# Kernel tuning notes

Measured on AMD Instinct MI355X. Metric: run time of the kernel, lower is better.

The kernel has to match this reference:

```python
import jax, jax.numpy as jnp
import numpy as np

D_MODEL = 256
D_INNER = 512   # expand=2
D_STATE = 16
D_CONV = 4
DT_RANK = 16    # ceil(d_model/16)
EPS = 1e-5


def _ln(x, g, b):
    m = x.mean(-1, keepdims=True)
    v = jnp.mean((x - m) ** 2, -1, keepdims=True)
    return (x - m) * jax.lax.rsqrt(v + EPS) * g + b


def _mamba(x, W_in, conv_w, conv_b, W_x, W_dt, b_dt, A_log, Dp, W_out):
    B, N, _ = x.shape
    xz = x @ W_in.T                               # [B,N,2*Di]
    xs, z = jnp.split(xz, 2, axis=-1)
    # depthwise causal conv1d, kernel D_CONV, left pad D_CONV-1
    xp = jnp.pad(xs, ((0, 0), (D_CONV - 1, 0), (0, 0)))
    xc = sum(xp[:, k:k + N, :] * conv_w[:, k] for k in range(D_CONV)) + conv_b
    xc = jax.nn.silu(xc)                          # [B,N,Di]
    dbl = xc @ W_x.T                              # [B,N,dt_rank+2*S]
    dt, Bm, Cm = jnp.split(dbl, [DT_RANK, DT_RANK + D_STATE], axis=-1)
    dt = jax.nn.softplus(dt @ W_dt.T + b_dt)      # [B,N,Di]
    A = -jnp.exp(A_log)                           # [Di,S]
    dA = jnp.exp(dt[..., None] * A)               # [B,N,Di,S]
    dBx = dt[..., None] * Bm[:, :, None, :] * xc[..., None]

    def step(h, inp):
        dA_t, dBx_t, c_t = inp                    # [B,Di,S],[B,Di,S],[B,S]
        h = dA_t * h + dBx_t
        y = jnp.einsum('bds,bs->bd', h, c_t)
        return h, y

    h0 = jnp.zeros((B, D_INNER, D_STATE), xs.dtype)
    _, ys = jax.lax.scan(step, h0, (dA.swapaxes(0, 1), dBx.swapaxes(0, 1), Cm.swapaxes(0, 1)))
    y = ys.swapaxes(0, 1) + Dp * xc
    y = y * jax.nn.silu(z)
    return y @ W_out.T                            # [B,N,d_model]


def setup_inputs() -> dict:
    key = jax.random.key(0)
    ks = jax.random.split(key, 24)
    g = lambda k, s, sc=0.02: jax.random.normal(k, s, jnp.float32) * sc
    inp = {}
    inp['input_states'] = jax.random.normal(ks[0], (1, 8192, D_MODEL), jnp.float32)
    inp['position_states'] = jax.random.normal(ks[1], (1, 8192, D_MODEL), jnp.float32)
    inp['W_in'] = g(ks[2], (2 * D_INNER, D_MODEL))
    inp['conv_w'] = g(ks[3], (D_INNER, D_CONV), 0.2)
    inp['conv_b'] = jnp.zeros((D_INNER,), jnp.float32)
    inp['W_x'] = g(ks[4], (DT_RANK + 2 * D_STATE, D_INNER))
    inp['W_dt'] = g(ks[5], (D_INNER, DT_RANK), 0.1)
    inp['b_dt'] = g(ks[6], (D_INNER,), 0.1)
    # S4D-real init: A_log = log(1..d_state) broadcast over channels
    inp['A_log'] = jnp.log(jnp.broadcast_to(jnp.arange(1, D_STATE + 1, dtype=jnp.float32), (D_INNER, D_STATE)))
    inp['Dp'] = jnp.ones((D_INNER,), jnp.float32)
    inp['W_out'] = g(ks[7], (D_MODEL, D_INNER))
    inp['W_lin'] = g(ks[8], (D_MODEL, D_MODEL))
    inp['b_lin'] = jnp.zeros((D_MODEL,), jnp.float32)
    inp['ln1_g'] = jnp.ones((D_MODEL,), jnp.float32)
    inp['ln1_b'] = jnp.zeros((D_MODEL,), jnp.float32)
    inp['W_exp'] = g(ks[9], (2 * D_MODEL, D_MODEL))
    inp['b_exp'] = jnp.zeros((2 * D_MODEL,), jnp.float32)
    inp['W_sq'] = g(ks[10], (D_MODEL, 2 * D_MODEL))
    inp['b_sq'] = jnp.zeros((D_MODEL,), jnp.float32)
    inp['ln2_g'] = jnp.ones((D_MODEL,), jnp.float32)
    inp['ln2_b'] = jnp.zeros((D_MODEL,), jnp.float32)
    return inp


def reference(input_states, position_states, W_in, conv_w, conv_b, W_x, W_dt, b_dt,
              A_log, Dp, W_out, W_lin, b_lin, ln1_g, ln1_b, W_exp, b_exp, W_sq, b_sq,
              ln2_g, ln2_b):
    h = _mamba(input_states, W_in, conv_w, conv_b, W_x, W_dt, b_dt, A_log, Dp, W_out)
    h = h @ W_lin.T + b_lin
    h = _ln(h + input_states, ln1_g, ln1_b)
    ff = jax.nn.relu(h @ W_exp.T + b_exp) @ W_sq.T + b_sq
    out = _ln(h + ff, ln2_g, ln2_b)
    # RPEMamba returns (hidden, input_states) as (states, attention_scores)
    return out, input_states
```

## Files before the change

### kernel.cpp

```cpp
#include <hip/hip_runtime.h>
#include <stdint.h>

#define NT 8192
#define DM 256
#define DI 512
#define DS 16
#define DR 16
#define NCH 256
#define LCH 32
#define NSUP 16
#define CPS 16

typedef __bf16 bf16_t;
typedef bf16_t bf16x8 __attribute__((ext_vector_type(8)));
typedef float f32x4 __attribute__((ext_vector_type(4)));

__device__ __forceinline__ unsigned short f2b(float f) {
    union { float f; unsigned int i; } v; v.f = f;
    unsigned int r = v.i + 0x7fffu + ((v.i >> 16) & 1u);
    return (unsigned short)(r >> 16);
}
__device__ __forceinline__ bf16x8 ld_frag_lds(const unsigned short* p) {
    union { uint4 u; bf16x8 b; } v;
    v.u = *(const uint4*)p;
    return v.b;
}
__device__ __forceinline__ void async16(const unsigned short* g, unsigned short* l) {
    __builtin_amdgcn_global_load_lds(
        (const __attribute__((address_space(1))) unsigned int*)g,
        (__attribute__((address_space(3))) unsigned int*)l, 16, 0, 0);
}

struct CvtArgs {
    const float* src[7];
    unsigned short* dst[7];
    int cnt[7];
    int total;
};
__global__ __launch_bounds__(256) void cvt_all(CvtArgs a) {
    int i = blockIdx.x * 256 + threadIdx.x;
    if (i >= a.total) return;
    #pragma unroll
    for (int s = 0; s < 7; s++) {
        if (i < a.cnt[s]) { a.dst[s][i] = f2b(a.src[s][i]); return; }
        i -= a.cnt[s];
    }
}

template<int BM, int BN, int FLAGS>
__global__ __launch_bounds__(256) void gemm_lds(
    const unsigned short* __restrict__ A, const unsigned short* __restrict__ B,
    int M, int N, int K,
    const float* __restrict__ bias, const float* __restrict__ resid,
    float* __restrict__ Cf, unsigned short* __restrict__ Cb)
{
    constexpr int MI = BM / 32;
    constexpr int NJ = BN / 32;
    __shared__ unsigned short sA[BM * 64];
    __shared__ unsigned short sB[BN * 64];
    const int tid = threadIdx.x;
    const int m0 = blockIdx.x * BM;
    const int n0 = blockIdx.y * BN;
    const int wave = tid >> 6, lane = tid & 63;
    const int wm = (wave & 1) * (BM / 2);
    const int wn = (wave >> 1) * (BN / 2);
    const int qm = lane >> 4, rm = lane & 15;

    f32x4 acc[MI][NJ];
    #pragma unroll
    for (int i = 0; i < MI; i++)
        #pragma unroll
        for (int j = 0; j < NJ; j++)
            #pragma unroll
            for (int r = 0; r < 4; r++) acc[i][j][r] = 0.f;

    const int sr = tid >> 3;
    const int sc = (tid & 7) * 8;

    for (int k0 = 0; k0 < K; k0 += 64) {
        __syncthreads();
        #pragma unroll
        for (int j = 0; j < BM / 32; j++) {
            int r = sr + j * 32;
            async16(A + (size_t)(m0 + r) * K + k0 + sc, &sA[r * 64 + sc]);
        }
        #pragma unroll
        for (int j = 0; j < BN / 32; j++) {
            int r = sr + j * 32;
            if (n0 + r < N)
                async16(B + (size_t)(n0 + r) * K + k0 + sc, &sB[r * 64 + sc]);
        }
        __syncthreads();
        #pragma unroll
        for (int ks = 0; ks < 64; ks += 32) {
            bf16x8 af[MI], bfr[NJ];
            #pragma unroll
            for (int i = 0; i < MI; i++)
                af[i] = ld_frag_lds(&sA[(wm + i * 16 + rm) * 64 + ks + qm * 8]);
            #pragma unroll
            for (int j = 0; j < NJ; j++)
                bfr[j] = ld_frag_lds(&sB[(wn + j * 16 + rm) * 64 + ks + qm * 8]);
            #pragma unroll
            for (int i = 0; i < MI; i++)
                #pragma unroll
                for (int j = 0; j < NJ; j++)
                    acc[i][j] = __builtin_amdgcn_mfma_f32_16x16x32_bf16(
                        af[i], bfr[j], acc[i][j], 0, 0, 0);
        }
    }

    #pragma unroll
    for (int i = 0; i < MI; i++) {
        int mrow = m0 + wm + i * 16 + qm * 4;
        #pragma unroll
        for (int j = 0; j < NJ; j++) {
            int ncol = n0 + wn + j * 16 + rm;
            if (ncol < N) {
                #pragma unroll
                for (int r = 0; r < 4; r++) {
                    float v = acc[i][j][r];
                    int mm = mrow + r;
                    if constexpr (FLAGS & 1) v += bias[ncol];
                    if constexpr (FLAGS & 4) v += resid[(size_t)mm * N + ncol];
                    if constexpr (FLAGS & 2) v = v > 0.f ? v : 0.f;
                    if constexpr (FLAGS & 8) Cf[(size_t)mm * N + ncol] = v;
                    if constexpr (FLAGS & 16) Cb[(size_t)mm * N + ncol] = f2b(v);
                }
            }
        }
    }
}

__global__ __launch_bounds__(256) void conv_silu(
    const float* __restrict__ xz, const float* __restrict__ cw,
    const float* __restrict__ cb, float* __restrict__ xc,
    unsigned short* __restrict__ xcb)
{
    int idx = blockIdx.x * 256 + threadIdx.x;
    int d = idx & (DI - 1), t = idx >> 9;
    float v = cb[d];
    #pragma unroll
    for (int k = 0; k < 4; k++) {
        int tt = t - 3 + k;
        if (tt >= 0) v += xz[(size_t)tt * 1024 + d] * cw[d * 4 + k];
    }
    float s = v / (1.f + __expf(-v));
    xc[idx] = s;
    xcb[idx] = f2b(s);
}

__global__ __launch_bounds__(256) void scan1(
    const float* __restrict__ dbl, const float* __restrict__ Wdt,
    const float* __restrict__ bdt, const float* __restrict__ xc,
    const float* __restrict__ A_log, float* __restrict__ dt,
    float* __restrict__ Ac, float* __restrict__ Bc)
{
    __shared__ float sD[LCH][DR];
    __shared__ float sB[LCH][DS];
    const int d = blockIdx.x * 256 + threadIdx.x;
    const int c = blockIdx.y;
    const int t0 = c * LCH;
    for (int e = threadIdx.x; e < LCH * 32; e += 256) {
        int tt = e >> 5, col = e & 31;
        float v = dbl[(size_t)(t0 + tt) * 48 + col];
        if (col < DR) sD[tt][col] = v; else sB[tt][col - DR] = v;
    }
    __syncthreads();
    float w[DR];
    #pragma unroll
    for (int j = 0; j < DR; j++) w[j] = Wdt[d * DR + j];
    const float bd = bdt[d];
    float A[DS], h[DS];
    #pragma unroll
    for (int s = 0; s < DS; s++) { A[s] = -__expf(A_log[d * DS + s]); h[s] = 0.f; }
    float sumdt = 0.f;
    for (int t = 0; t < LCH; t++) {
        float accd = bd;
        #pragma unroll
        for (int j = 0; j < DR; j++) accd += sD[t][j] * w[j];
        float dtv = accd > 20.f ? accd : log1pf(__expf(accd));
        dt[(size_t)(t0 + t) * DI + d] = dtv;
        float xcv = xc[(size_t)(t0 + t) * DI + d];
        float dtx = dtv * xcv;
        sumdt += dtv;
        #pragma unroll
        for (int s = 0; s < DS; s++)
            h[s] = __expf(dtv * A[s]) * h[s] + dtx * sB[t][s];
    }
    #pragma unroll
    for (int s = 0; s < DS; s++) {
        size_t off = ((size_t)c * DS + s) * DI + d;
        Ac[off] = __expf(sumdt * A[s]);
        Bc[off] = h[s];
    }
}

__global__ __launch_bounds__(256) void scan2a(
    const float* __restrict__ Ac, const float* __restrict__ Bc,
    float* __restrict__ Ap, float* __restrict__ Hl,
    float* __restrict__ Es, float* __restrict__ Ds)
{
    int p = blockIdx.x * 256 + threadIdx.x;
    int j = blockIdx.y;
    float h = 0.f, P = 1.f;
    for (int cc = 0; cc < CPS; cc++) {
        size_t off = (size_t)(j * CPS + cc) * 8192 + p;
        Hl[off] = h; Ap[off] = P;
        float a = Ac[off];
        h = a * h + Bc[off];
        P *= a;
    }
    Es[(size_t)j * 8192 + p] = h;
    Ds[(size_t)j * 8192 + p] = P;
}

__global__ __launch_bounds__(256) void scan2b(
    const float* __restrict__ Es, const float* __restrict__ Ds,
    float* __restrict__ Ss)
{
    int p = blockIdx.x * 256 + threadIdx.x;
    float S = 0.f;
    for (int j = 0; j < NSUP; j++) {
        Ss[(size_t)j * 8192 + p] = S;
        S = Ds[(size_t)j * 8192 + p] * S + Es[(size_t)j * 8192 + p];
    }
}

__global__ __launch_bounds__(256) void scan3(
    const float* __restrict__ dt, const float* __restrict__ xc,
    const float* __restrict__ xz, const float* __restrict__ dbl,
    const float* __restrict__ A_log, const float* __restrict__ Dp,
    const float* __restrict__ Ap, const float* __restrict__ Hl,
    const float* __restrict__ Ss, unsigned short* __restrict__ ygb)
{
    __shared__ float sB[LCH][DS];
    __shared__ float sC[LCH][DS];
    const int d = blockIdx.x * 256 + threadIdx.x;
    const int c = blockIdx.y;
    const int jsup = c >> 4;
    const int t0 = c * LCH;
    for (int e = threadIdx.x; e < LCH * 32; e += 256) {
        int tt = e >> 5, col = e & 31;
        float v = dbl[(size_t)(t0 + tt) * 48 + DR + col];
        if (col < DS) sB[tt][col] = v; else sC[tt][col - DS] = v;
    }
    __syncthreads();
    float A[DS], h[DS];
    #pragma unroll
    for (int s = 0; s < DS; s++) {
        A[s] = -__expf(A_log[d * DS + s]);
        size_t off = (size_t)c * 8192 + s * DI + d;
        h[s] = Ap[off] * Ss[(size_t)jsup * 8192 + s * DI + d] + Hl[off];
    }
    float dpv = Dp[d];
    for (int t = 0; t < LCH; t++) {
        float dtv = dt[(size_t)(t0 + t) * DI + d];
        float xcv = xc[(size_t)(t0 + t) * DI + d];
        float zv  = xz[(size_t)(t0 + t) * 1024 + DI + d];
        float dtx = dtv * xcv;
        float y = 0.f;
        #pragma unroll
        for (int s = 0; s < DS; s++) {
            h[s] = __expf(dtv * A[s]) * h[s] + dtx * sB[t][s];
            y += h[s] * sC[t][s];
        }
        float sz = zv / (1.f + __expf(-zv));
        ygb[(size_t)(t0 + t) * DI + d] = f2b((y + dpv * xcv) * sz);
    }
}

__global__ __launch_bounds__(256) void lnorm(
    const float* __restrict__ X, const float* __restrict__ X2,
    const float* __restrict__ g, const float* __restrict__ b,
    float* __restrict__ outf, unsigned short* __restrict__ outb)
{
    int wave = threadIdx.x >> 6, lane = threadIdx.x & 63;
    int row = blockIdx.x * 4 + wave;
    const float* x = X + (size_t)row * DM;
    float v[4];
    #pragma unroll
    for (int i = 0; i < 4; i++) {
        int col = lane + i * 64;
        v[i] = x[col];
        if (X2) v[i] += X2[(size_t)row * DM + col];
    }
    float s = v[0] + v[1] + v[2] + v[3];
    float s2 = v[0]*v[0] + v[1]*v[1] + v[2]*v[2] + v[3]*v[3];
    #pragma unroll
    for (int m = 1; m < 64; m <<= 1) {
        s  += __shfl_xor(s, m, 64);
        s2 += __shfl_xor(s2, m, 64);
    }
    float mean = s * (1.f / DM);
    float var = s2 * (1.f / DM) - mean * mean;
    float inv = rsqrtf(var + 1e-5f);
    #pragma unroll
    for (int i = 0; i < 4; i++) {
        int col = lane + i * 64;
        float o = (v[i] - mean) * inv * g[col] + b[col];
        if (outf) outf[(size_t)row * DM + col] = o;
        if (outb) outb[(size_t)row * DM + col] = f2b(o);
    }
}

static constexpr size_t OFF_XZ    = 0;
static constexpr size_t OFF_XC    = 33554432;
static constexpr size_t OFF_XCB   = 50331648;
static constexpr size_t OFF_DBL   = 58720256;
static constexpr size_t OFF_DT    = 60293120;
static constexpr size_t OFF_AC    = 77070336;
static constexpr size_t OFF_BC    = 85458944;
static constexpr size_t OFF_HL    = 93847552;
static constexpr size_t OFF_AP    = 102236160;
static constexpr size_t OFF_YGB   = 110624768;
static constexpr size_t OFF_XB    = 119013376;
static constexpr size_t OFF_ES    = 123207680;
static constexpr size_t OFF_DS2   = 123731968;
static constexpr size_t OFF_SS    = 124256256;
static constexpr size_t OFF_WINB  = 124780544;
static constexpr size_t OFF_WXB   = 125304832;
static constexpr size_t OFF_WOUTB = 125353984;
static constexpr size_t OFF_WLINB = 125616128;
static constexpr size_t OFF_WEXPB = 125747200;
static constexpr size_t OFF_WSQB  = 126009344;
static constexpr size_t OFF_H1B   = OFF_XZ;
static constexpr size_t OFF_H2    = OFF_XZ + 4194304;
static constexpr size_t OFF_HLN   = OFF_XZ + 12582912;
static constexpr size_t OFF_HLNB  = OFF_XZ + 20971520;
static constexpr size_t OFF_FF1B  = OFF_DT;
static constexpr size_t OFF_FF2   = OFF_DT + 8388608;

extern "C" void kernel_launch(void* const* d_in, const int* in_sizes, int n_in,
                              void* d_out, int out_size, void* d_ws, size_t ws_size,
                              hipStream_t stream)
{
    const float* x      = (const float*)d_in[0];
    const float* W_in   = (const float*)d_in[2];
    const float* conv_w = (const float*)d_in[3];
    const float* conv_b = (const float*)d_in[4];
    const float* W_x    = (const float*)d_in[5];
    const float* W_dt   = (const float*)d_in[6];
    const float* b_dt   = (const float*)d_in[7];
    const float* A_log  = (const float*)d_in[8];
    const float* Dp     = (const float*)d_in[9];
    const float* W_out  = (const float*)d_in[10];
    const float* W_lin  = (const float*)d_in[11];
    const float* b_lin  = (const float*)d_in[12];
    const float* ln1_g  = (const float*)d_in[13];
    const float* ln1_b  = (const float*)d_in[14];
    const float* W_exp  = (const float*)d_in[15];
    const float* b_exp  = (const float*)d_in[16];
    const float* W_sq   = (const float*)d_in[17];
    const float* b_sq   = (const float*)d_in[18];
    const float* ln2_g  = (const float*)d_in[19];
    const float* ln2_b  = (const float*)d_in[20];

    char* ws = (char*)d_ws;
    float* xz   = (float*)(ws + OFF_XZ);
    float* xc   = (float*)(ws + OFF_XC);
    unsigned short* xcb = (unsigned short*)(ws + OFF_XCB);
    float* dbl  = (float*)(ws + OFF_DBL);
    float* dtf  = (float*)(ws + OFF_DT);
    float* Ac   = (float*)(ws + OFF_AC);
    float* Bc   = (float*)(ws + OFF_BC);
    float* Hl   = (float*)(ws + OFF_HL);
    float* Ap   = (float*)(ws + OFF_AP);
    float* Es   = (float*)(ws + OFF_ES);
    float* Ds   = (float*)(ws + OFF_DS2);
    float* Ss   = (float*)(ws + OFF_SS);
    unsigned short* ygb   = (unsigned short*)(ws + OFF_YGB);
    unsigned short* xb    = (unsigned short*)(ws + OFF_XB);
    unsigned short* winb  = (unsigned short*)(ws + OFF_WINB);
    unsigned short* wxb   = (unsigned short*)(ws + OFF_WXB);
    unsigned short* woutb = (unsigned short*)(ws + OFF_WOUTB);
    unsigned short* wlinb = (unsigned short*)(ws + OFF_WLINB);
    unsigned short* wexpb = (unsigned short*)(ws + OFF_WEXPB);
    unsigned short* wsqb  = (unsigned short*)(ws + OFF_WSQB);
    unsigned short* h1b   = (unsigned short*)(ws + OFF_H1B);
    float* h2   = (float*)(ws + OFF_H2);
    float* hln  = (float*)(ws + OFF_HLN);
    unsigned short* hlnb  = (unsigned short*)(ws + OFF_HLNB);
    unsigned short* ff1b  = (unsigned short*)(ws + OFF_FF1B);
    float* ff2  = (float*)(ws + OFF_FF2);
    float* outp = (float*)d_out;

    CvtArgs ca;
    ca.src[0] = x;     ca.dst[0] = xb;    ca.cnt[0] = NT * DM;
    ca.src[1] = W_in;  ca.dst[1] = winb;  ca.cnt[1] = 1024 * DM;
    ca.src[2] = W_x;   ca.dst[2] = wxb;   ca.cnt[2] = 48 * DI;
    ca.src[3] = W_out; ca.dst[3] = woutb; ca.cnt[3] = DM * DI;
    ca.src[4] = W_lin; ca.dst[4] = wlinb; ca.cnt[4] = DM * DM;
    ca.src[5] = W_exp; ca.dst[5] = wexpb; ca.cnt[5] = DI * DM;
    ca.src[6] = W_sq;  ca.dst[6] = wsqb;  ca.cnt[6] = DM * DI;
    ca.total = ca.cnt[0]+ca.cnt[1]+ca.cnt[2]+ca.cnt[3]+ca.cnt[4]+ca.cnt[5]+ca.cnt[6];
    cvt_all<<<(ca.total + 255) / 256, 256, 0, stream>>>(ca);

    gemm_lds<128,128,8><<<dim3(64, 8), 256, 0, stream>>>(xb, winb, NT, 1024, DM,
                                                         nullptr, nullptr, xz, nullptr);
    conv_silu<<<NT * DI / 256, 256, 0, stream>>>(xz, conv_w, conv_b, xc, xcb);
    gemm_lds<128,64,8><<<dim3(64, 1), 256, 0, stream>>>(xcb, wxb, NT, 48, DI,
                                                        nullptr, nullptr, dbl, nullptr);
    scan1<<<dim3(2, NCH), 256, 0, stream>>>(dbl, W_dt, b_dt, xc, A_log, dtf, Ac, Bc);
    scan2a<<<dim3(32, NSUP), 256, 0, stream>>>(Ac, Bc, Ap, Hl, Es, Ds);
    scan2b<<<32, 256, 0, stream>>>(Es, Ds, Ss);
    scan3<<<dim3(2, NCH), 256, 0, stream>>>(dtf, xc, xz, dbl, A_log, Dp, Ap, Hl, Ss, ygb);
    gemm_lds<64,128,16><<<dim3(128, 2), 256, 0, stream>>>(ygb, woutb, NT, DM, DI,
                                                          nullptr, nullptr, nullptr, h1b);
    gemm_lds<64,128,1|4|8><<<dim3(128, 2), 256, 0, stream>>>(h1b, wlinb, NT, DM, DM,
                                                             b_lin, x, h2, nullptr);
    lnorm<<<NT / 4, 256, 0, stream>>>(h2, nullptr, ln1_g, ln1_b, hln, hlnb);
    gemm_lds<128,128,1|2|16><<<dim3(64, 4), 256, 0, stream>>>(hlnb, wexpb, NT, DI, DM,
                                                              b_exp, nullptr, nullptr, ff1b);
    gemm_lds<64,128,1|8><<<dim3(128, 2), 256, 0, stream>>>(ff1b, wsqb, NT, DM, DI,
                                                           b_sq, nullptr, ff2, nullptr);
    lnorm<<<NT / 4, 256, 0, stream>>>(hln, ff2, ln2_g, ln2_b, outp, nullptr);
    hipMemcpyAsync(outp + (size_t)NT * DM, x, (size_t)NT * DM * sizeof(float),
                   hipMemcpyDeviceToDevice, stream);
}
```

Baseline: 292.0 us.

## Recompute conv/dt inside scan kernels, halve chunk length, fold output copy into layernorm

The scan kernels now recompute the causal conv+SiLU and the dt projection/softplus from xz and dbl instead of reading fp32 xc and dt buffers, which removes those intermediate arrays and their global traffic. Chunk length drops from 32 to 16, doubling the number of chunks and super-chunks, which gives more parallel blocks but makes the scan2 stages longer. The passthrough copy of input_states is moved into the final layernorm kernel, replacing a separate memcpy. The cost is redundant arithmetic in both scan passes and larger Ac/Bc/Hl/Ap buffers.

Result: no change. 289.4 us (-0.9%).

```diff
diff --git a/kernel.cpp b/kernel.cpp
--- a/kernel.cpp
+++ b/kernel.cpp
@@ -6,9 +6,9 @@
 #define DI 512
 #define DS 16
 #define DR 16
-#define NCH 256
-#define LCH 32
-#define NSUP 16
+#define NCH 512
+#define LCH 16
+#define NSUP 32
 #define CPS 16
 
 typedef __bf16 bf16_t;
@@ -29,6 +29,12 @@
     __builtin_amdgcn_global_load_lds(
         (const __attribute__((address_space(1))) unsigned int*)g,
         (__attribute__((address_space(3))) unsigned int*)l, 16, 0, 0);
+}
+__device__ __forceinline__ float fast_softplus(float x) {
+    return x > 20.f ? x : __logf(1.f + __expf(x));
+}
+__device__ __forceinline__ float silu(float x) {
+    return x / (1.f + __expf(-x));
 }
 
 struct CvtArgs {
@@ -131,10 +137,9 @@
     }
 }
 
-__global__ __launch_bounds__(256) void conv_silu(
+__global__ __launch_bounds__(256) void conv_silu_b(
     const float* __restrict__ xz, const float* __restrict__ cw,
-    const float* __restrict__ cb, float* __restrict__ xc,
-    unsigned short* __restrict__ xcb)
+    const float* __restrict__ cb, unsigned short* __restrict__ xcb)
 {
     int idx = blockIdx.x * 256 + threadIdx.x;
     int d = idx & (DI - 1), t = idx >> 9;
@@ -144,48 +149,59 @@
         int tt = t - 3 + k;
         if (tt >= 0) v += xz[(size_t)tt * 1024 + d] * cw[d * 4 + k];
     }
-    float s = v / (1.f + __expf(-v));
-    xc[idx] = s;
-    xcb[idx] = f2b(s);
-}
-
-__global__ __launch_bounds__(256) void scan1(
-    const float* __restrict__ dbl, const float* __restrict__ Wdt,
-    const float* __restrict__ bdt, const float* __restrict__ xc,
-    const float* __restrict__ A_log, float* __restrict__ dt,
+    xcb[idx] = f2b(silu(v));
+}
+
+__global__ __launch_bounds__(256, 4) void scan1(
+    const float* __restrict__ xz, const float* __restrict__ cw,
+    const float* __restrict__ cbp, const float* __restrict__ dbl,
+    const float* __restrict__ Wdt, const float* __restrict__ bdt,
+    const float* __restrict__ A_log,
     float* __restrict__ Ac, float* __restrict__ Bc)
 {
-    __shared__ float sD[LCH][DR];
-    __shared__ float sB[LCH][DS];
+    __shared__ float sR[LCH * 48];
     const int d = blockIdx.x * 256 + threadIdx.x;
     const int c = blockIdx.y;
     const int t0 = c * LCH;
-    for (int e = threadIdx.x; e < LCH * 32; e += 256) {
-        int tt = e >> 5, col = e & 31;
-        float v = dbl[(size_t)(t0 + tt) * 48 + col];
-        if (col < DR) sD[tt][col] = v; else sB[tt][col - DR] = v;
+    {
+        const float4* src = (const float4*)(dbl + (size_t)t0 * 48);
+        if (threadIdx.x < 192) ((float4*)sR)[threadIdx.x] = src[threadIdx.x];
     }
     __syncthreads();
-    float w[DR];
+    const float cw0 = cw[d*4], cw1 = cw[d*4+1], cw2 = cw[d*4+2], cw3 = cw[d*4+3];
+    const float cb = cbp[d];
+    const float* xzp = xz + d;
+    float x0 = (t0 >= 3) ? xzp[(size_t)(t0-3) * 1024] : 0.f;
+    float x1 = (t0 >= 2) ? xzp[(size_t)(t0-2) * 1024] : 0.f;
+    float x2 = (t0 >= 1) ? xzp[(size_t)(t0-1) * 1024] : 0.f;
+    float w[DR], A[DS], h[DS];
     #pragma unroll
     for (int j = 0; j < DR; j++) w[j] = Wdt[d * DR + j];
     const float bd = bdt[d];
-    float A[DS], h[DS];
     #pragma unroll
     for (int s = 0; s < DS; s++) { A[s] = -__expf(A_log[d * DS + s]); h[s] = 0.f; }
     float sumdt = 0.f;
+    #pragma unroll 4
     for (int t = 0; t < LCH; t++) {
+        float x3 = xzp[(size_t)(t0 + t) * 1024];
+        float cv = cb + x0 * cw0 + x1 * cw1 + x2 * cw2 + x3 * cw3;
+        x0 = x1; x1 = x2; x2 = x3;
+        float xcv = silu(cv);
+        const float* r = &sR[t * 48];
+        float4 rd[4], rb[4];
+        #pragma unroll
+        for (int k = 0; k < 4; k++) { rd[k] = ((const float4*)r)[k]; rb[k] = ((const float4*)r)[4 + k]; }
         float accd = bd;
         #pragma unroll
-        for (int j = 0; j < DR; j++) accd += sD[t][j] * w[j];
-        float dtv = accd > 20.f ? accd : log1pf(__expf(accd));
-        dt[(size_t)(t0 + t) * DI + d] = dtv;
-        float xcv = xc[(size_t)(t0 + t) * DI + d];
+        for (int k = 0; k < 4; k++)
+            accd += rd[k].x * w[4*k] + rd[k].y * w[4*k+1] + rd[k].z * w[4*k+2] + rd[k].w * w[4*k+3];
+        float dtv = fast_softplus(accd);
+        sumdt += dtv;
         float dtx = dtv * xcv;
-        sumdt += dtv;
+        const float* bptr = (const float*)rb;
         #pragma unroll
         for (int s = 0; s < DS; s++)
-            h[s] = __expf(dtv * A[s]) * h[s] + dtx * sB[t][s];
+            h[s] = __expf(dtv * A[s]) * h[s] + dtx * bptr[s];
     }
     #pragma unroll
     for (int s = 0; s < DS; s++) {
@@ -226,53 +242,80 @@
     }
 }
 
-__global__ __launch_bounds__(256) void scan3(
-    const float* __restrict__ dt, const float* __restrict__ xc,
-    const float* __restrict__ xz, const float* __restrict__ dbl,
-    const float* __restrict__ A_log, const float* __restrict__ Dp,
+__global__ __launch_bounds__(256, 4) void scan3(
+    const float* __restrict__ xz, const float* __restrict__ cw,
+    const float* __restrict__ cbp, const float* __restrict__ dbl,
+    const float* __restrict__ Wdt, const float* __restrict__ bdt,
+    const float* __restrict__ A_log, const float* __restrict__ Dpp,
     const float* __restrict__ Ap, const float* __restrict__ Hl,
     const float* __restrict__ Ss, unsigned short* __restrict__ ygb)
 {
-    __shared__ float sB[LCH][DS];
-    __shared__ float sC[LCH][DS];
+    __shared__ float sR[LCH * 48];
     const int d = blockIdx.x * 256 + threadIdx.x;
     const int c = blockIdx.y;
-    const int jsup = c >> 4;
+    const int jsup = c / CPS;
     const int t0 = c * LCH;
-    for (int e = threadIdx.x; e < LCH * 32; e += 256) {
-        int tt = e >> 5, col = e & 31;
-        float v = dbl[(size_t)(t0 + tt) * 48 + DR + col];
-        if (col < DS) sB[tt][col] = v; else sC[tt][col - DS] = v;
+    {
+        const float4* src = (const float4*)(dbl + (size_t)t0 * 48);
+        if (threadIdx.x < 192) ((float4*)sR)[threadIdx.x] = src[threadIdx.x];
     }
     __syncthreads();
-    float A[DS], h[DS];
+    const float cw0 = cw[d*4], cw1 = cw[d*4+1], cw2 = cw[d*4+2], cw3 = cw[d*4+3];
+    const float cb = cbp[d];
+    const float* xzp = xz + d;
+    const float* zp  = xz + DI + d;
+    float x0 = (t0 >= 3) ? xzp[(size_t)(t0-3) * 1024] : 0.f;
+    float x1 = (t0 >= 2) ? xzp[(size_t)(t0-2) * 1024] : 0.f;
+    float x2 = (t0 >= 1) ? xzp[(size_t)(t0-1) * 1024] : 0.f;
+    float w[DR], A[DS], h[DS];
+    #pragma unroll
+    for (int j = 0; j < DR; j++) w[j] = Wdt[d * DR + j];
+    const float bd = bdt[d];
+    const float dpv = Dpp[d];
     #pragma unroll
     for (int s = 0; s < DS; s++) {
         A[s] = -__expf(A_log[d * DS + s]);
         size_t off = (size_t)c * 8192 + s * DI + d;
         h[s] = Ap[off] * Ss[(size_t)jsup * 8192 + s * DI + d] + Hl[off];
     }
-    float dpv = Dp[d];
+    #pragma unroll 4
     for (int t = 0; t < LCH; t++) {
-        float dtv = dt[(size_t)(t0 + t) * DI + d];
-        float xcv = xc[(size_t)(t0 + t) * DI + d];
-        float zv  = xz[(size_t)(t0 + t) * 1024 + DI + d];
+        float x3 = xzp[(size_t)(t0 + t) * 1024];
+        float zv = zp[(size_t)(t0 + t) * 1024];
+        float cv = cb + x0 * cw0 + x1 * cw1 + x2 * cw2 + x3 * cw3;
+        x0 = x1; x1 = x2; x2 = x3;
+        float xcv = silu(cv);
+        const float* r = &sR[t * 48];
+        float4 rd[4], rb[4], rc[4];
+        #pragma unroll
+        for (int k = 0; k < 4; k++) {
+            rd[k] = ((const float4*)r)[k];
+            rb[k] = ((const float4*)r)[4 + k];
+            rc[k] = ((const float4*)r)[8 + k];
+        }
+        float accd = bd;
+        #pragma unroll
+        for (int k = 0; k < 4; k++)
+            accd += rd[k].x * w[4*k] + rd[k].y * w[4*k+1] + rd[k].z * w[4*k+2] + rd[k].w * w[4*k+3];
+        float dtv = fast_softplus(accd);
         float dtx = dtv * xcv;
+        const float* bptr = (const float*)rb;
+        const float* cptr = (const float*)rc;
         float y = 0.f;
         #pragma unroll
         for (int s = 0; s < DS; s++) {
-            h[s] = __expf(dtv * A[s]) * h[s] + dtx * sB[t][s];
-            y += h[s] * sC[t][s];
-        }
-        float sz = zv / (1.f + __expf(-zv));
-        ygb[(size_t)(t0 + t) * DI + d] = f2b((y + dpv * xcv) * sz);
+            h[s] = __expf(dtv * A[s]) * h[s] + dtx * bptr[s];
+            y += h[s] * cptr[s];
+        }
+        ygb[(size_t)(t0 + t) * DI + d] = f2b((y + dpv * xcv) * silu(zv));
     }
 }
 
 __global__ __launch_bounds__(256) void lnorm(
     const float* __restrict__ X, const float* __restrict__ X2,
     const float* __restrict__ g, const float* __restrict__ b,
-    float* __restrict__ outf, unsigned short* __restrict__ outb)
+    float* __restrict__ outf, unsigned short* __restrict__ outb,
+    const float* __restrict__ csrc, float* __restrict__ cdst)
 {
     int wave = threadIdx.x >> 6, lane = threadIdx.x & 63;
     int row = blockIdx.x * 4 + wave;
@@ -283,6 +326,13 @@
         int col = lane + i * 64;
         v[i] = x[col];
         if (X2) v[i] += X2[(size_t)row * DM + col];
+    }
+    if (cdst) {
+        #pragma unroll
+        for (int i = 0; i < 4; i++) {
+            int col = lane + i * 64;
+            cdst[(size_t)row * DM + col] = csrc[(size_t)row * DM + col];
+        }
     }
     float s = v[0] + v[1] + v[2] + v[3];
     float s2 = v[0]*v[0] + v[1]*v[1] + v[2]*v[2] + v[3]*v[3];
@@ -304,31 +354,29 @@
 }
 
 static constexpr size_t OFF_XZ    = 0;
-static constexpr size_t OFF_XC    = 33554432;
-static constexpr size_t OFF_XCB   = 50331648;
-static constexpr size_t OFF_DBL   = 58720256;
-static constexpr size_t OFF_DT    = 60293120;
-static constexpr size_t OFF_AC    = 77070336;
-static constexpr size_t OFF_BC    = 85458944;
-static constexpr size_t OFF_HL    = 93847552;
-static constexpr size_t OFF_AP    = 102236160;
-static constexpr size_t OFF_YGB   = 110624768;
-static constexpr size_t OFF_XB    = 119013376;
-static constexpr size_t OFF_ES    = 123207680;
-static constexpr size_t OFF_DS2   = 123731968;
-static constexpr size_t OFF_SS    = 124256256;
-static constexpr size_t OFF_WINB  = 124780544;
-static constexpr size_t OFF_WXB   = 125304832;
-static constexpr size_t OFF_WOUTB = 125353984;
-static constexpr size_t OFF_WLINB = 125616128;
-static constexpr size_t OFF_WEXPB = 125747200;
-static constexpr size_t OFF_WSQB  = 126009344;
-static constexpr size_t OFF_H1B   = OFF_XZ;
-static constexpr size_t OFF_H2    = OFF_XZ + 4194304;
-static constexpr size_t OFF_HLN   = OFF_XZ + 12582912;
-static constexpr size_t OFF_HLNB  = OFF_XZ + 20971520;
-static constexpr size_t OFF_FF1B  = OFF_DT;
-static constexpr size_t OFF_FF2   = OFF_DT + 8388608;
+static constexpr size_t OFF_XCB   = 33554432;
+static constexpr size_t OFF_DBL   = 41943040;
+static constexpr size_t OFF_AC    = 43515904;
+static constexpr size_t OFF_BC    = 60293120;
+static constexpr size_t OFF_HL    = 77070336;
+static constexpr size_t OFF_AP    = 93847552;
+static constexpr size_t OFF_ES    = 110624768;
+static constexpr size_t OFF_DS2   = 111673344;
+static constexpr size_t OFF_SS    = 112721920;
+static constexpr size_t OFF_YGB   = 113770496;
+static constexpr size_t OFF_XB    = 122159104;
+static constexpr size_t OFF_WINB  = 126353408;
+static constexpr size_t OFF_WXB   = 126877696;
+static constexpr size_t OFF_WOUTB = 126926848;
+static constexpr size_t OFF_WLINB = 127188992;
+static constexpr size_t OFF_WEXPB = 127320064;
+static constexpr size_t OFF_WSQB  = 127582208;
+static constexpr size_t OFF_H1B   = OFF_AC;
+static constexpr size_t OFF_H2    = OFF_AC + 4194304;
+static constexpr size_t OFF_HLN   = OFF_BC;
+static constexpr size_t OFF_HLNB  = OFF_BC + 8388608;
+static constexpr size_t OFF_FF1B  = OFF_HL;
+static constexpr size_t OFF_FF2   = OFF_AP;
 
 extern "C" void kernel_launch(void* const* d_in, const int* in_sizes, int n_in,
                               void* d_out, int out_size, void* d_ws, size_t ws_size,
@@ -357,10 +405,8 @@
 
     char* ws = (char*)d_ws;
     float* xz   = (float*)(ws + OFF_XZ);
-    float* xc   = (float*)(ws + OFF_XC);
     unsigned short* xcb = (unsigned short*)(ws + OFF_XCB);
     float* dbl  = (float*)(ws + OFF_DBL);
-    float* dtf  = (float*)(ws + OFF_DT);
     float* Ac   = (float*)(ws + OFF_AC);
     float* Bc   = (float*)(ws + OFF_BC);
     float* Hl   = (float*)(ws + OFF_HL);
@@ -397,23 +443,25 @@
 
     gemm_lds<128,128,8><<<dim3(64, 8), 256, 0, stream>>>(xb, winb, NT, 1024, DM,
                                                          nullptr, nullptr, xz, nullptr);
-    conv_silu<<<NT * DI / 256, 256, 0, stream>>>(xz, conv_w, conv_b, xc, xcb);
+    conv_silu_b<<<NT * DI / 256, 256, 0, stream>>>(xz, conv_w, conv_b, xcb);
     gemm_lds<128,64,8><<<dim3(64, 1), 256, 0, stream>>>(xcb, wxb, NT, 48, DI,
                                                         nullptr, nullptr, dbl, nullptr);
-    scan1<<<dim3(2, NCH), 256, 0, stream>>>(dbl, W_dt, b_dt, xc, A_log, dtf, Ac, Bc);
+    scan1<<<dim3(2, NCH), 256, 0, stream>>>(xz, conv_w, conv_b, dbl, W_dt, b_dt,
+                                            A_log, Ac, Bc);
     scan2a<<<dim3(32, NSUP), 256, 0, stream>>>(Ac, Bc, Ap, Hl, Es, Ds);
     scan2b<<<32, 256, 0, stream>>>(Es, Ds, Ss);
-    scan3<<<dim3(2, NCH), 256, 0, stream>>>(dtf, xc, xz, dbl, A_log, Dp, Ap, Hl, Ss, ygb);
+    scan3<<<dim3(2, NCH), 256, 0, stream>>>(xz, conv_w, conv_b, dbl, W_dt, b_dt,
+                                            A_log, Dp, Ap, Hl, Ss, ygb);
     gemm_lds<64,128,16><<<dim3(128, 2), 256, 0, stream>>>(ygb, woutb, NT, DM, DI,
                                                           nullptr, nullptr, nullptr, h1b);
     gemm_lds<64,128,1|4|8><<<dim3(128, 2), 256, 0, stream>>>(h1b, wlinb, NT, DM, DM,
                                                              b_lin, x, h2, nullptr);
-    lnorm<<<NT / 4, 256, 0, stream>>>(h2, nullptr, ln1_g, ln1_b, hln, hlnb);
+    lnorm<<<NT / 4, 256, 0, stream>>>(h2, nullptr, ln1_g, ln1_b, hln, hlnb,
+                                      nullptr, nullptr);
     gemm_lds<128,128,1|2|16><<<dim3(64, 4), 256, 0, stream>>>(hlnb, wexpb, NT, DI, DM,
                                                               b_exp, nullptr, nullptr, ff1b);
     gemm_lds<64,128,1|8><<<dim3(128, 2), 256, 0, stream>>>(ff1b, wsqb, NT, DM, DI,
                                                            b_sq, nullptr, ff2, nullptr);
-    lnorm<<<NT / 4, 256, 0, stream>>>(hln, ff2, ln2_g, ln2_b, outp, nullptr);
-    hipMemcpyAsync(outp + (size_t)NT * DM, x, (size_t)NT * DM * sizeof(float),
-                   hipMemcpyDeviceToDevice, stream);
-}
+    lnorm<<<NT / 4, 256, 0, stream>>>(hln, ff2, ln2_g, ln2_b, outp, nullptr,
+                                      x, outp + (size_t)NT * DM);
+}
```
